# Kernel optimization log

Hardware: AMD Instinct MI355X
Metric: run time of the kernel (lower is better)

## Reference

```python
import jax, jax.numpy as jnp
import numpy as np

H = 2        # num_heads
C = 128      # in_channels
K_ORDER = 4
BETA = 0.5


def _gcn_conv(x, row, col, deg_inv, n):
    # x: [N, H, C]; adj_t = D^{-1} A^T where A[row, col] = 1
    # (adj_t @ x)[c] = deg_inv[c] * sum_{e: col_e == c} x[row_e]
    msg = x[row]  # [E, H, C]
    agg = jax.ops.segment_sum(msg, col, num_segments=n)  # [N, H, C]
    return agg * deg_inv[:, None, None]


def _attn_conv(qs, ks, vs):
    # linear (kernelized) attention, non-block path
    n = qs.shape[0]
    kvs = jnp.einsum('lhm,lhd->hmd', ks, vs)            # [H, C, C]
    qkvs = jnp.einsum('nhm,hmd->nhd', qs, kvs)          # [N, H, C]
    vs_sum = vs.sum(axis=0)                             # [H, C]
    num = qkvs + vs_sum[None, :, :]
    ks_sum = ks.sum(axis=0)                             # [H, C]
    qks_sum = jnp.einsum('nhm,hm->nh', qs, ks_sum)[:, :, None]  # [N, H, 1]
    den = qks_sum + jnp.asarray(n, qs.dtype)
    return num / den


def setup_inputs() -> dict:
    key = jax.random.key(0)
    ks = jax.random.split(key, 8)
    N, E = 100000, 1600000
    x = jax.random.normal(ks[0], (N, C), jnp.float32)
    edge_index = jax.random.randint(ks[1], (2, E), 0, N, jnp.int64)
    s_in = 1.0 / np.sqrt(C)
    s_out = 1.0 / np.sqrt(H * C * (K_ORDER + 1))
    Wq_w = jax.random.normal(ks[2], (C, H * C), jnp.float32) * s_in
    Wq_b = jax.random.normal(ks[3], (H * C,), jnp.float32) * s_in
    Wk_w = jax.random.normal(ks[4], (C, H * C), jnp.float32) * s_in
    Wk_b = jax.random.normal(ks[5], (H * C,), jnp.float32) * s_in
    Wo_w = jax.random.normal(ks[6], (H * C * (K_ORDER + 1), C), jnp.float32) * s_out
    Wo_b = jax.random.normal(ks[7], (C,), jnp.float32) * s_out
    return {"x": x, "edge_index": edge_index, "Wq_w": Wq_w, "Wq_b": Wq_b,
            "Wk_w": Wk_w, "Wk_b": Wk_b, "Wo_w": Wo_w, "Wo_b": Wo_b}


def reference(x, edge_index, Wq_w, Wq_b, Wk_w, Wk_b, Wo_w, Wo_b):
    n = x.shape[0]
    row, col = edge_index[0], edge_index[1]
    # normalized adjacency D^{-1} A^T (pow(-1.0) in the source, not -0.5)
    deg = jax.ops.segment_sum(jnp.ones(row.shape[0], x.dtype), col, num_segments=n)
    deg_inv = jnp.where(deg > 0, 1.0 / deg, 0.0)

    query = (x @ Wq_w + Wq_b).reshape(n, H, C)
    key = (x @ Wk_w + Wk_b).reshape(n, H, C)
    qs = query / jnp.linalg.norm(query, axis=2, keepdims=True)
    ks = key / jnp.linalg.norm(key, axis=2, keepdims=True)

    x0 = jnp.broadcast_to(x[:, None, :], (n, H, C))  # [N, H, C]
    terms = [x0]
    for _ in range(K_ORDER):
        prev = terms[-1]
        gcn_i = _gcn_conv(prev, row, col, deg_inv, n)
        attn_i = _attn_conv(qs, ks, prev)
        terms.append(BETA * gcn_i + attn_i)
    xcat = jnp.concatenate(terms, axis=-1)  # [N, H, C*(K+1)]
    xcat = xcat.reshape(n, H * C * (K_ORDER + 1))
    return (xcat @ Wo_w + Wo_b) / H
```

## Files before the change

### kernel.cpp

```cpp
#include <hip/hip_runtime.h>

#define THREADS 256
#define NB 512
#define SEGCAP 6144

typedef __attribute__((ext_vector_type(8))) short short8;
typedef __attribute__((ext_vector_type(4))) float f32x4;

__device__ __forceinline__ float bf2f(unsigned short u) {
    union { unsigned int i; float f; } v;
    v.i = ((unsigned int)u) << 16;
    return v.f;
}
__device__ __forceinline__ unsigned short f2bf(float f) {
    union { float f; unsigned int i; } v;
    v.f = f;
    unsigned int r = (v.i + 0x7FFFu + ((v.i >> 16) & 1u)) >> 16;
    return (unsigned short)r;
}
__device__ __forceinline__ float4 ld4f(const float* p) {
    return *reinterpret_cast<const float4*>(p);
}
__device__ __forceinline__ float4 ld4f(const unsigned short* p) {
    ushort4 u = *reinterpret_cast<const ushort4*>(p);
    return make_float4(bf2f(u.x), bf2f(u.y), bf2f(u.z), bf2f(u.w));
}

__device__ __forceinline__ int edge_get(const int* base, int E, int mode, int which, int e) {
    size_t idx = (size_t)which * (size_t)E + (size_t)e;
    return mode ? base[2 * idx] : base[idx];
}

__global__ __launch_bounds__(256) void k_detect(const int* __restrict__ e, int E,
                                                int* __restrict__ mode) {
    __shared__ int nz;
    if (threadIdx.x == 0) nz = 0;
    __syncthreads();
    int lim = 2 * E;
    if (lim > 8192) lim = 8192;
    for (int i = 1 + 2 * (int)threadIdx.x; i < lim; i += 512)
        if (e[i] != 0) nz = 1;
    __syncthreads();
    if (threadIdx.x == 0) *mode = (nz == 0) ? 1 : 0;
}

__global__ __launch_bounds__(256) void k_hist(const int* __restrict__ eb, int E,
                                              const int* __restrict__ mode, int N, int CW, int epb,
                                              int* __restrict__ gcnt) {
    __shared__ int hist[NB];
    for (int i = threadIdx.x; i < NB; i += 256) hist[i] = 0;
    __syncthreads();
    int m = *mode;
    int e0 = blockIdx.x * epb;
    int e1 = min(e0 + epb, E);
    for (int e = e0 + threadIdx.x; e < e1; e += 256) {
        int c = edge_get(eb, E, m, 1, e);
        if ((unsigned)c < (unsigned)N) atomicAdd(&hist[c / CW], 1);
    }
    __syncthreads();
    for (int i = threadIdx.x; i < NB; i += 256)
        if (hist[i]) atomicAdd(&gcnt[i], hist[i]);
}

__global__ __launch_bounds__(NB) void k_bscan(const int* __restrict__ gcnt,
                                              int* __restrict__ gbase, int* __restrict__ gcursor) {
    __shared__ int s[NB];
    int t = threadIdx.x;
    int v = gcnt[t];
    s[t] = v;
    __syncthreads();
    for (int off = 1; off < NB; off <<= 1) {
        int add = (t >= off) ? s[t - off] : 0;
        __syncthreads();
        s[t] += add;
        __syncthreads();
    }
    gbase[t] = s[t] - v;
    gcursor[t] = s[t] - v;
}

__global__ __launch_bounds__(256) void k_part(const int* __restrict__ eb, int E,
                                              const int* __restrict__ mode, int N, int CW, int epb,
                                              int* __restrict__ gcursor, uint2* __restrict__ ebuf) {
    __shared__ int hist[NB];
    __shared__ int base[NB];
    for (int i = threadIdx.x; i < NB; i += 256) hist[i] = 0;
    __syncthreads();
    int m = *mode;
    int e0 = blockIdx.x * epb;
    int e1 = min(e0 + epb, E);
    for (int e = e0 + threadIdx.x; e < e1; e += 256) {
        int c = edge_get(eb, E, m, 1, e);
        if ((unsigned)c < (unsigned)N) atomicAdd(&hist[c / CW], 1);
    }
    __syncthreads();
    for (int i = threadIdx.x; i < NB; i += 256) {
        int h = hist[i];
        base[i] = h ? atomicAdd(&gcursor[i], h) : 0;
        hist[i] = 0;
    }
    __syncthreads();
    for (int e = e0 + threadIdx.x; e < e1; e += 256) {
        int c = edge_get(eb, E, m, 1, e);
        if ((unsigned)c < (unsigned)N) {
            int r = edge_get(eb, E, m, 0, e);
            if ((unsigned)r >= (unsigned)N) r = 0;
            int b = c / CW;
            int li = atomicAdd(&hist[b], 1);
            ebuf[(size_t)base[b] + li] = make_uint2((unsigned)r, (unsigned)c);
        }
    }
}

__global__ __launch_bounds__(256) void k_build(const uint2* __restrict__ ebuf,
                                               const int* __restrict__ gbase,
                                               const int* __restrict__ gcnt, int N, int CW,
                                               int* __restrict__ cnt, int* __restrict__ offs,
                                               float* __restrict__ deg_inv, int* __restrict__ csr) {
    __shared__ int hist[256];
    __shared__ int pfx[256];
    __shared__ int seg[SEGCAP];
    const int b = blockIdx.x;
    const int col0 = b * CW;
    const int ncols = min(CW, N - col0);
    if (ncols <= 0) return;
    const int ebase = gbase[b], ecnt = gcnt[b];
    const int t = threadIdx.x;
    for (int i = t; i < 256; i += 256) hist[i] = 0;
    __syncthreads();
    for (int e = t; e < ecnt; e += 256) {
        uint2 rc = ebuf[(size_t)ebase + e];
        atomicAdd(&hist[rc.y - col0], 1);
    }
    __syncthreads();
    int v = (t < ncols) ? hist[t] : 0;
    pfx[t] = v;
    __syncthreads();
    for (int off = 1; off < 256; off <<= 1) {
        int add = (t >= off) ? pfx[t - off] : 0;
        __syncthreads();
        pfx[t] += add;
        __syncthreads();
    }
    int excl = pfx[t] - v;
    if (t < ncols) {
        cnt[col0 + t] = v;
        offs[col0 + t] = ebase + excl;
        deg_inv[col0 + t] = (v > 0) ? 1.0f / (float)v : 0.0f;
    }
    __syncthreads();
    if (t < 256) hist[t] = (t < ncols) ? excl : 0;
    __syncthreads();
    if (ecnt <= SEGCAP) {
        for (int e = t; e < ecnt; e += 256) {
            uint2 rc = ebuf[(size_t)ebase + e];
            int li = atomicAdd(&hist[rc.y - col0], 1);
            seg[li] = (int)rc.x;
        }
        __syncthreads();
        for (int e = t; e < ecnt; e += 256) csr[(size_t)ebase + e] = seg[e];
    } else {
        for (int e = t; e < ecnt; e += 256) {
            uint2 rc = ebuf[(size_t)ebase + e];
            int li = atomicAdd(&hist[rc.y - col0], 1);
            csr[(size_t)ebase + li] = (int)rc.x;
        }
    }
}

__global__ __launch_bounds__(256) void k_prep_wqk(const float* __restrict__ Wq,
                                                  const float* __restrict__ Wk,
                                                  unsigned short* __restrict__ WqkT) {
    int i = blockIdx.x * 256 + threadIdx.x;
    if (i < 512 * 128) {
        int oc = i >> 7, k = i & 127;
        float v = (oc < 256) ? Wq[k * 256 + oc] : Wk[k * 256 + (oc - 256)];
        WqkT[i] = f2bf(v);
    }
}

__global__ __launch_bounds__(256) void k_prep_wo(const float* __restrict__ Wo,
                                                 unsigned short* __restrict__ WoT) {
    int i = blockIdx.x * 256 + threadIdx.x;
    if (i < 1280 * 128) {
        int r = i >> 7, j = i & 127;
        WoT[(size_t)j * 1280 + r] = f2bf(Wo[i]);
    }
}

__global__ __launch_bounds__(256) void k_proj(const float* __restrict__ x,
                                              const unsigned short* __restrict__ WqkT,
                                              const float* __restrict__ bq,
                                              const float* __restrict__ bk,
                                              unsigned short* __restrict__ qs,
                                              unsigned short* __restrict__ ks, int N) {
    __shared__ unsigned short xs[64 * 128];
    __shared__ unsigned short os[64 * 256];
    const int t = threadIdx.x;
    const int n0 = blockIdx.x * 64;
#pragma unroll
    for (int i = 0; i < 4; i++) {
        int chunk = i * 256 + t;
        int r = chunk >> 4, c0 = (chunk & 15) * 8;
        float4 a0 = make_float4(0.f, 0.f, 0.f, 0.f), a1 = a0;
        if (n0 + r < N) {
            a0 = ld4f(&x[(size_t)(n0 + r) * 128 + c0]);
            a1 = ld4f(&x[(size_t)(n0 + r) * 128 + c0 + 4]);
        }
        short8 v = {(short)f2bf(a0.x), (short)f2bf(a0.y), (short)f2bf(a0.z), (short)f2bf(a0.w),
                    (short)f2bf(a1.x), (short)f2bf(a1.y), (short)f2bf(a1.z), (short)f2bf(a1.w)};
        int byte = r * 256 + ((c0 * 2) ^ ((r & 7) << 4));
        *reinterpret_cast<short8*>(reinterpret_cast<char*>(xs) + byte) = v;
    }
    __syncthreads();
    const int w = t >> 6, l = t & 63, lrow = l & 15, lhi = l >> 4;
    f32x4 acc[4][8];
    const f32x4 fz = {0.f, 0.f, 0.f, 0.f};
#pragma unroll
    for (int mt = 0; mt < 4; mt++)
#pragma unroll
        for (int nt = 0; nt < 8; nt++) acc[mt][nt] = fz;

    for (int kk = 0; kk < 4; kk++) {
        int kb = kk * 32 + lhi * 8;
        short8 af[4];
#pragma unroll
        for (int mt = 0; mt < 4; mt++) {
            int r = mt * 16 + lrow;
            af[mt] = *reinterpret_cast<const short8*>(
                reinterpret_cast<const char*>(xs) + r * 256 + ((kb * 2) ^ ((r & 7) << 4)));
        }
#pragma unroll
        for (int nt = 0; nt < 8; nt++) {
            int oc = w * 128 + nt * 16 + lrow;
            short8 bf = *reinterpret_cast<const short8*>(&WqkT[(size_t)oc * 128 + kb]);
#pragma unroll
            for (int mt = 0; mt < 4; mt++)
                acc[mt][nt] = __builtin_amdgcn_mfma_f32_16x16x32_bf16(af[mt], bf, acc[mt][nt], 0, 0, 0);
        }
    }
#pragma unroll
    for (int nt = 0; nt < 8; nt++) {
        int oc = w * 128 + nt * 16 + lrow;
        float b = (oc < 256) ? bq[oc] : bk[oc - 256];
#pragma unroll
        for (int mt = 0; mt < 4; mt++)
#pragma unroll
            for (int reg = 0; reg < 4; reg++) acc[mt][nt][reg] += b;
    }
    const int hc = (w & 1) * 128;
    float rv[4][4];
#pragma unroll
    for (int mt = 0; mt < 4; mt++) {
        float ss[4] = {0.f, 0.f, 0.f, 0.f};
#pragma unroll
        for (int nt = 0; nt < 8; nt++)
#pragma unroll
            for (int reg = 0; reg < 4; reg++) ss[reg] += acc[mt][nt][reg] * acc[mt][nt][reg];
#pragma unroll
        for (int m_ = 1; m_ < 16; m_ <<= 1)
#pragma unroll
            for (int reg = 0; reg < 4; reg++) ss[reg] += __shfl_xor(ss[reg], m_);
#pragma unroll
        for (int reg = 0; reg < 4; reg++) rv[mt][reg] = rsqrtf(ss[reg]);
    }
    for (int pass = 0; pass < 2; pass++) {
        if ((w >> 1) == pass) {
#pragma unroll
            for (int mt = 0; mt < 4; mt++)
#pragma unroll
                for (int reg = 0; reg < 4; reg++) {
                    int r = mt * 16 + lhi * 4 + reg;
#pragma unroll
                    for (int nt = 0; nt < 8; nt++)
                        os[r * 256 + hc + nt * 16 + lrow] = f2bf(acc[mt][nt][reg] * rv[mt][reg]);
                }
        }
        __syncthreads();
        unsigned short* dstg = pass ? ks : qs;
#pragma unroll
        for (int i = 0; i < 8; i++) {
            int chunk = i * 256 + t;
            int r = chunk >> 5, c = (chunk & 31) * 8;
            int n = n0 + r;
            if (n < N)
                *reinterpret_cast<short8*>(&dstg[(size_t)n * 256 + c]) =
                    *reinterpret_cast<const short8*>(&os[r * 256 + c]);
        }
        __syncthreads();
    }
}

__global__ __launch_bounds__(256) void k_colsum(const unsigned short* __restrict__ ks, int N,
                                                float* __restrict__ part) {
    const int t = threadIdx.x;
    const int stride = (N + 255) >> 8;
    int r0 = blockIdx.x * stride;
    int rend = min(r0 + stride, N);
    float s = 0.f;
    for (int n = r0; n < rend; n++) s += bf2f(ks[(size_t)n * 256 + t]);
    part[blockIdx.x * 256 + t] = s;
}

__global__ __launch_bounds__(256) void k_colsum2(const float* __restrict__ part,
                                                 float* __restrict__ ks_sum) {
    const int t = threadIdx.x;
    float s = 0.f;
    for (int b = 0; b < 256; b++) s += part[b * 256 + t];
    ks_sum[t] = s;
}

__global__ __launch_bounds__(256) void k_den(const unsigned short* __restrict__ qs,
                                             const float* __restrict__ ks_sum,
                                             float* __restrict__ den, int N) {
    int w = threadIdx.x >> 6, lane = threadIdx.x & 63;
    int n = blockIdx.x * 4 + w;
    if (n >= N) return;
    float4 q = ld4f(&qs[(size_t)n * 256 + lane * 4]);
    float4 kv = *reinterpret_cast<const float4*>(&ks_sum[lane * 4]);
    float s = q.x * kv.x + q.y * kv.y + q.z * kv.z + q.w * kv.w;
#pragma unroll
    for (int off = 1; off < 32; off <<= 1) s += __shfl_xor(s, off);
    if ((lane & 31) == 0) den[n * 2 + (lane >> 5)] = s + (float)N;
}

__device__ __forceinline__ short8 frag_ld(const unsigned short* tile, int kb, int col) {
    const char* b = reinterpret_cast<const char*>(tile);
    int cb = (col * 2) ^ (((kb >> 3) & 3) << 5);
    short8 r;
#pragma unroll
    for (int i = 0; i < 8; i++)
        r[i] = (short)*reinterpret_cast<const unsigned short*>(b + (kb + i) * 512 + cb);
    return r;
}

template <typename TV>
__global__ __launch_bounds__(256) void k_kvs2(const unsigned short* __restrict__ ks,
                                              const TV* __restrict__ vs, int vstride, int vmask,
                                              float* __restrict__ partial,
                                              float* __restrict__ pvsum, int rows_per, int N) {
    __shared__ unsigned short kt[32 * 256];
    __shared__ unsigned short vt[32 * 256];
    __shared__ float vred[8][256];
    const int t = threadIdx.x;
    const int w = t >> 6, l = t & 63, lrow = l & 15, lhi = l >> 4;
    const int h = w >> 1, mhalf = w & 1;
    const int r0 = blockIdx.x * rows_per;
    const int rend = min(r0 + rows_per, N);

    const f32x4 fz = {0.f, 0.f, 0.f, 0.f};
    f32x4 acc[4][8];
#pragma unroll
    for (int mt = 0; mt < 4; mt++)
#pragma unroll
        for (int nt = 0; nt < 8; nt++) acc[mt][nt] = fz;
    float vsum8[8] = {0.f, 0.f, 0.f, 0.f, 0.f, 0.f, 0.f, 0.f};

    for (int c0 = r0; c0 < rend; c0 += 32) {
#pragma unroll
        for (int i = 0; i < 4; i++) {
            int chunk = i * 256 + t;
            int n = chunk >> 5, cc = (chunk & 31) * 8;
            short8 v = {0, 0, 0, 0, 0, 0, 0, 0};
            if (c0 + n < rend)
                v = *reinterpret_cast<const short8*>(&ks[(size_t)(c0 + n) * 256 + cc]);
            *reinterpret_cast<short8*>(reinterpret_cast<char*>(kt) + n * 512 +
                                       ((cc * 2) ^ (((n >> 3) & 3) << 5))) = v;
        }
#pragma unroll
        for (int i = 0; i < 4; i++) {
            int chunk = i * 256 + t;
            int n = chunk >> 5, cc = (chunk & 31) * 8;
            float4 a0 = make_float4(0.f, 0.f, 0.f, 0.f), a1 = a0;
            if (c0 + n < rend) {
                a0 = ld4f(&vs[(size_t)(c0 + n) * vstride + (cc & vmask)]);
                a1 = ld4f(&vs[(size_t)(c0 + n) * vstride + ((cc + 4) & vmask)]);
            }
            unsigned short u0 = f2bf(a0.x), u1 = f2bf(a0.y), u2 = f2bf(a0.z), u3 = f2bf(a0.w);
            unsigned short u4 = f2bf(a1.x), u5 = f2bf(a1.y), u6 = f2bf(a1.z), u7 = f2bf(a1.w);
            vsum8[0] += bf2f(u0); vsum8[1] += bf2f(u1); vsum8[2] += bf2f(u2); vsum8[3] += bf2f(u3);
            vsum8[4] += bf2f(u4); vsum8[5] += bf2f(u5); vsum8[6] += bf2f(u6); vsum8[7] += bf2f(u7);
            short8 v = {(short)u0, (short)u1, (short)u2, (short)u3,
                        (short)u4, (short)u5, (short)u6, (short)u7};
            *reinterpret_cast<short8*>(reinterpret_cast<char*>(vt) + n * 512 +
                                       ((cc * 2) ^ (((n >> 3) & 3) << 5))) = v;
        }
        __syncthreads();
        {
            int kb = lhi * 8;
            short8 af[4];
#pragma unroll
            for (int mt = 0; mt < 4; mt++)
                af[mt] = frag_ld(vt, kb, h * 128 + mhalf * 64 + mt * 16 + lrow);
#pragma unroll
            for (int nt = 0; nt < 8; nt++) {
                short8 bf = frag_ld(kt, kb, h * 128 + nt * 16 + lrow);
#pragma unroll
                for (int mt = 0; mt < 4; mt++)
                    acc[mt][nt] =
                        __builtin_amdgcn_mfma_f32_16x16x32_bf16(af[mt], bf, acc[mt][nt], 0, 0, 0);
            }
        }
        __syncthreads();
    }
    float* pb = &partial[((size_t)blockIdx.x * 2 + h) * 16384];
#pragma unroll
    for (int mt = 0; mt < 4; mt++)
#pragma unroll
        for (int reg = 0; reg < 4; reg++) {
            int c_local = mhalf * 64 + mt * 16 + lhi * 4 + reg;
#pragma unroll
            for (int nt = 0; nt < 8; nt++) pb[c_local * 128 + nt * 16 + lrow] = acc[mt][nt][reg];
        }
    {
        int cc = (t & 31) * 8;
#pragma unroll
        for (int j = 0; j < 8; j++) vred[t >> 5][cc + j] = vsum8[j];
        __syncthreads();
        float s = 0.f;
#pragma unroll
        for (int r = 0; r < 8; r++) s += vred[r][t];
        pvsum[blockIdx.x * 256 + t] = s;
    }
}

__global__ __launch_bounds__(256) void k_kvred(const float* __restrict__ partial,
                                               const float* __restrict__ pvsum, int S,
                                               unsigned short* __restrict__ kvsT,
                                               float* __restrict__ vs_sum) {
    if (blockIdx.x == 128) {
        int c = threadIdx.x;
        float s = 0.f;
        for (int i = 0; i < S; i++) s += pvsum[i * 256 + c];
        vs_sum[c] = s;
        return;
    }
    int e = blockIdx.x * 256 + threadIdx.x;
    float s = 0.f;
    for (int i = 0; i < S; i++) s += partial[(size_t)i * 32768 + e];
    kvsT[e] = f2bf(s);
}

__global__ __launch_bounds__(256) void k_gather2(const unsigned short* __restrict__ prev,
                                                 const int* __restrict__ csr_src,
                                                 const int* __restrict__ offs,
                                                 const int* __restrict__ cnt,
                                                 const float* __restrict__ deg_inv,
                                                 unsigned short* __restrict__ cur, int N) {
    const int w = threadIdx.x >> 6, l = threadIdx.x & 63;
    int n = blockIdx.x * 4 + w;
    if (n >= N) return;
    const int start = offs[n], d = cnt[n];
    int e = start;
    const int eend = start + d;
    float a0 = 0.f, a1 = 0.f, a2 = 0.f, a3 = 0.f;
    const int co = l * 4;
    for (; e + 8 <= eend; e += 8) {
        int s[8];
#pragma unroll
        for (int i = 0; i < 8; i++) s[i] = csr_src[e + i];
        ushort4 u[8];
#pragma unroll
        for (int i = 0; i < 8; i++)
            u[i] = *reinterpret_cast<const ushort4*>(&prev[(size_t)s[i] * 256 + co]);
#pragma unroll
        for (int i = 0; i < 8; i++) {
            a0 += bf2f(u[i].x); a1 += bf2f(u[i].y); a2 += bf2f(u[i].z); a3 += bf2f(u[i].w);
        }
    }
    for (; e < eend; e++) {
        ushort4 u = *reinterpret_cast<const ushort4*>(&prev[(size_t)csr_src[e] * 256 + co]);
        a0 += bf2f(u.x); a1 += bf2f(u.y); a2 += bf2f(u.z); a3 += bf2f(u.w);
    }
    float sc = 0.5f * deg_inv[n];
    ushort4 o;
    o.x = f2bf(a0 * sc); o.y = f2bf(a1 * sc); o.z = f2bf(a2 * sc); o.w = f2bf(a3 * sc);
    *reinterpret_cast<ushort4*>(&cur[(size_t)n * 256 + co]) = o;
}

__global__ __launch_bounds__(256) void k_gather2f(const float* __restrict__ prev,
                                                  const int* __restrict__ csr_src,
                                                  const int* __restrict__ offs,
                                                  const int* __restrict__ cnt,
                                                  const float* __restrict__ deg_inv,
                                                  unsigned short* __restrict__ cur, int N) {
    const int w = threadIdx.x >> 6, l = threadIdx.x & 63;
    int n = blockIdx.x * 4 + w;
    if (n >= N) return;
    const int start = offs[n], d = cnt[n];
    int e = start;
    const int eend = start + d;
    float a0 = 0.f, a1 = 0.f;
    const int co = l * 2;
    for (; e + 8 <= eend; e += 8) {
        int s[8];
#pragma unroll
        for (int i = 0; i < 8; i++) s[i] = csr_src[e + i];
        float2 u[8];
#pragma unroll
        for (int i = 0; i < 8; i++)
            u[i] = *reinterpret_cast<const float2*>(&prev[(size_t)s[i] * 128 + co]);
#pragma unroll
        for (int i = 0; i < 8; i++) { a0 += u[i].x; a1 += u[i].y; }
    }
    for (; e < eend; e++) {
        float2 u = *reinterpret_cast<const float2*>(&prev[(size_t)csr_src[e] * 128 + co]);
        a0 += u.x; a1 += u.y;
    }
    float sc = 0.5f * deg_inv[n];
    ushort2 o;
    o.x = f2bf(a0 * sc); o.y = f2bf(a1 * sc);
    *reinterpret_cast<ushort2*>(&cur[(size_t)n * 256 + co]) = o;
    *reinterpret_cast<ushort2*>(&cur[(size_t)n * 256 + 128 + co]) = o;
}

__global__ __launch_bounds__(256) void k_att_out(const unsigned short* __restrict__ qs,
                                                 const unsigned short* __restrict__ kvsT,
                                                 const float* __restrict__ vs_sum,
                                                 const float* __restrict__ den,
                                                 unsigned short* __restrict__ cur,
                                                 const unsigned short* __restrict__ WoT,
                                                 float* __restrict__ out, int tblk, int N) {
    __shared__ unsigned short sm[64 * 256];
    const int t = threadIdx.x;
    const int n0 = blockIdx.x * 64;
#pragma unroll
    for (int i = 0; i < 8; i++) {
        int chunk = i * 256 + t;
        int r = chunk >> 5, c0 = (chunk & 31) * 8;
        short8 v = {0, 0, 0, 0, 0, 0, 0, 0};
        if (n0 + r < N) v = *reinterpret_cast<const short8*>(&qs[(size_t)(n0 + r) * 256 + c0]);
        *reinterpret_cast<short8*>(reinterpret_cast<char*>(sm) + r * 512 +
                                   ((c0 * 2) ^ ((r & 7) << 4))) = v;
    }
    __syncthreads();
    const int w = t >> 6, l = t & 63, lrow = l & 15, lhi = l >> 4;
    const int h = w >> 1, jh = w & 1;
    const f32x4 fz = {0.f, 0.f, 0.f, 0.f};
    f32x4 acc[4][4];
#pragma unroll
    for (int mt = 0; mt < 4; mt++)
#pragma unroll
        for (int nt = 0; nt < 4; nt++) acc[mt][nt] = fz;

    for (int kk = 0; kk < 4; kk++) {
        int kb = kk * 32 + lhi * 8;
        short8 af[4];
#pragma unroll
        for (int mt = 0; mt < 4; mt++) {
            int r = mt * 16 + lrow;
            af[mt] = *reinterpret_cast<const short8*>(
                reinterpret_cast<const char*>(sm) + r * 512 +
                (((h * 128 + kb) * 2) ^ ((r & 7) << 4)));
        }
#pragma unroll
        for (int nt = 0; nt < 4; nt++) {
            int c = jh * 64 + nt * 16 + lrow;
            short8 bf = *reinterpret_cast<const short8*>(&kvsT[((size_t)h * 128 + c) * 128 + kb]);
#pragma unroll
            for (int mt = 0; mt < 4; mt++)
                acc[mt][nt] = __builtin_amdgcn_mfma_f32_16x16x32_bf16(af[mt], bf, acc[mt][nt], 0, 0, 0);
        }
    }
    __syncthreads();
#pragma unroll
    for (int i = 0; i < 8; i++) {
        int chunk = i * 256 + t;
        int r = chunk >> 5, c0 = (chunk & 31) * 8;
        short8 v = {0, 0, 0, 0, 0, 0, 0, 0};
        if (n0 + r < N) v = *reinterpret_cast<const short8*>(&cur[(size_t)(n0 + r) * 256 + c0]);
        *reinterpret_cast<short8*>(reinterpret_cast<char*>(sm) + r * 512 +
                                   ((c0 * 2) ^ ((r & 7) << 4))) = v;
    }
    __syncthreads();
#pragma unroll
    for (int mt = 0; mt < 4; mt++) {
#pragma unroll
        for (int reg = 0; reg < 4; reg++) {
            int r = mt * 16 + lhi * 4 + reg;
            int n = n0 + r;
            if (n < N) {
                float idn = 1.0f / den[n * 2 + h];
#pragma unroll
                for (int nt = 0; nt < 4; nt++) {
                    int c = h * 128 + jh * 64 + nt * 16 + lrow;
                    unsigned short* sp = reinterpret_cast<unsigned short*>(
                        reinterpret_cast<char*>(sm) + r * 512 + ((c * 2) ^ ((r & 7) << 4)));
                    float v = bf2f(*sp) + (acc[mt][nt][reg] + vs_sum[c]) * idn;
                    *sp = f2bf(v);
                }
            }
        }
    }
    __syncthreads();
#pragma unroll
    for (int i = 0; i < 8; i++) {
        int chunk = i * 256 + t;
        int r = chunk >> 5, c0 = (chunk & 31) * 8;
        int n = n0 + r;
        if (n < N)
            *reinterpret_cast<short8*>(&cur[(size_t)n * 256 + c0]) =
                *reinterpret_cast<const short8*>(reinterpret_cast<const char*>(sm) + r * 512 +
                                                 ((c0 * 2) ^ ((r & 7) << 4)));
    }
    __syncthreads();
    f32x4 acc2[4][2];
#pragma unroll
    for (int mt = 0; mt < 4; mt++)
#pragma unroll
        for (int nt = 0; nt < 2; nt++) acc2[mt][nt] = fz;
    for (int kk = 0; kk < 8; kk++) {
        int kb = kk * 32 + lhi * 8;
        short8 af[4];
#pragma unroll
        for (int mt = 0; mt < 4; mt++) {
            int r = mt * 16 + lrow;
            af[mt] = *reinterpret_cast<const short8*>(
                reinterpret_cast<const char*>(sm) + r * 512 + ((kb * 2) ^ ((r & 7) << 4)));
        }
        int woff = (kb >> 7) * 640 + tblk * 128 + (kb & 127);
#pragma unroll
        for (int nt = 0; nt < 2; nt++) {
            int j = w * 32 + nt * 16 + lrow;
            short8 bf = *reinterpret_cast<const short8*>(&WoT[(size_t)j * 1280 + woff]);
#pragma unroll
            for (int mt = 0; mt < 4; mt++)
                acc2[mt][nt] = __builtin_amdgcn_mfma_f32_16x16x32_bf16(af[mt], bf, acc2[mt][nt], 0, 0, 0);
        }
    }
#pragma unroll
    for (int nt = 0; nt < 2; nt++) {
        int j = w * 32 + nt * 16 + lrow;
#pragma unroll
        for (int mt = 0; mt < 4; mt++)
#pragma unroll
            for (int reg = 0; reg < 4; reg++) {
                int n = n0 + mt * 16 + lhi * 4 + reg;
                if (n < N) out[(size_t)n * 128 + j] += 0.5f * acc2[mt][nt][reg];
            }
    }
}

__global__ __launch_bounds__(256) void k_out0(const float* __restrict__ x,
                                              const unsigned short* __restrict__ WoT,
                                              const float* __restrict__ Wo_b,
                                              float* __restrict__ out, int N) {
    __shared__ unsigned short sm[64 * 256];
    const int t = threadIdx.x;
    const int n0 = blockIdx.x * 64;
#pragma unroll
    for (int i = 0; i < 8; i++) {
        int chunk = i * 256 + t;
        int r = chunk >> 5, c0 = (chunk & 31) * 8, cs = c0 & 127;
        float4 a0 = make_float4(0.f, 0.f, 0.f, 0.f), a1 = a0;
        if (n0 + r < N) {
            a0 = ld4f(&x[(size_t)(n0 + r) * 128 + cs]);
            a1 = ld4f(&x[(size_t)(n0 + r) * 128 + cs + 4]);
        }
        short8 v = {(short)f2bf(a0.x), (short)f2bf(a0.y), (short)f2bf(a0.z), (short)f2bf(a0.w),
                    (short)f2bf(a1.x), (short)f2bf(a1.y), (short)f2bf(a1.z), (short)f2bf(a1.w)};
        *reinterpret_cast<short8*>(reinterpret_cast<char*>(sm) + r * 512 +
                                   ((c0 * 2) ^ ((r & 7) << 4))) = v;
    }
    __syncthreads();
    const int w = t >> 6, l = t & 63, lrow = l & 15, lhi = l >> 4;
    const f32x4 fz = {0.f, 0.f, 0.f, 0.f};
    f32x4 acc2[4][2];
#pragma unroll
    for (int mt = 0; mt < 4; mt++)
#pragma unroll
        for (int nt = 0; nt < 2; nt++) acc2[mt][nt] = fz;
    for (int kk = 0; kk < 8; kk++) {
        int kb = kk * 32 + lhi * 8;
        short8 af[4];
#pragma unroll
        for (int mt = 0; mt < 4; mt++) {
            int r = mt * 16 + lrow;
            af[mt] = *reinterpret_cast<const short8*>(
                reinterpret_cast<const char*>(sm) + r * 512 + ((kb * 2) ^ ((r & 7) << 4)));
        }
        int woff = (kb >> 7) * 640 + (kb & 127);
#pragma unroll
        for (int nt = 0; nt < 2; nt++) {
            int j = w * 32 + nt * 16 + lrow;
            short8 bf = *reinterpret_cast<const short8*>(&WoT[(size_t)j * 1280 + woff]);
#pragma unroll
            for (int mt = 0; mt < 4; mt++)
                acc2[mt][nt] = __builtin_amdgcn_mfma_f32_16x16x32_bf16(af[mt], bf, acc2[mt][nt], 0, 0, 0);
        }
    }
#pragma unroll
    for (int nt = 0; nt < 2; nt++) {
        int j = w * 32 + nt * 16 + lrow;
        float b = Wo_b[j];
#pragma unroll
        for (int mt = 0; mt < 4; mt++)
#pragma unroll
            for (int reg = 0; reg < 4; reg++) {
                int n = n0 + mt * 16 + lhi * 4 + reg;
                if (n < N) out[(size_t)n * 128 + j] = 0.5f * (acc2[mt][nt][reg] + b);
            }
    }
}

extern "C" void kernel_launch(void* const* d_in, const int* in_sizes, int n_in,
                              void* d_out, int out_size, void* d_ws, size_t ws_size,
                              hipStream_t stream) {
    const int N = in_sizes[0] / 128;
    const int E = in_sizes[1] / 2;
    const float* x = (const float*)d_in[0];
    const int* eraw = (const int*)d_in[1];
    const float* Wq_w = (const float*)d_in[2];
    const float* Wq_b = (const float*)d_in[3];
    const float* Wk_w = (const float*)d_in[4];
    const float* Wk_b = (const float*)d_in[5];
    const float* Wo_w = (const float*)d_in[6];
    const float* Wo_b = (const float*)d_in[7];
    float* out = (float*)d_out;

    char* p = (char*)d_ws;
    auto alloc = [&](size_t bytes) -> void* {
        void* r = (void*)p;
        p += (bytes + 255) & ~(size_t)255;
        return r;
    };
    unsigned short* qs = (unsigned short*)alloc((size_t)N * 256 * 2);
    unsigned short* ks = (unsigned short*)alloc((size_t)N * 256 * 2);
    unsigned short* bufA = (unsigned short*)alloc((size_t)N * 256 * 2);
    unsigned short* bufB = (unsigned short*)alloc((size_t)N * 256 * 2);
    float* deg_inv = (float*)alloc((size_t)N * 4);
    float* den = (float*)alloc((size_t)N * 2 * 4);
    float* ks_sum = (float*)alloc(256 * 4);
    float* vs_sum = (float*)alloc(256 * 4);
    float* colpart = (float*)alloc(256 * 256 * 4);
    unsigned short* WqkT = (unsigned short*)alloc(512 * 128 * 2);
    unsigned short* WoT = (unsigned short*)alloc(1280 * 128 * 2);
    unsigned short* kvsTb = (unsigned short*)alloc(32768 * 2);
    int* cnt = (int*)alloc((size_t)N * 4);
    int* offs = (int*)alloc((size_t)N * 4);
    int* gcnt = (int*)alloc(NB * 4);
    int* gbase = (int*)alloc(NB * 4);
    int* gcursor = (int*)alloc(NB * 4);
    int* mode = (int*)alloc(256);
    int* csr = (int*)alloc((size_t)E * 4);
    uint2* ebuf = (uint2*)alloc((size_t)E * 8);

    size_t used = (size_t)(p - (char*)d_ws);
    size_t rem = (ws_size > used + (1 << 20)) ? ws_size - used - (1 << 20) : 0;
    int S = (int)(rem / (32768 * 4 + 1024));
    if (S > 256) S = 256;
    if (S < 8) S = 8;
    float* partial = (float*)alloc((size_t)S * 32768 * 4);
    float* pvsum = (float*)alloc((size_t)S * 256 * 4);
    const int rows_per = (N + S - 1) / S;

    const int CW = (N + NB - 1) / NB;
    const int EBLK = 256;
    const int epb = (E + EBLK - 1) / EBLK;

    hipMemsetAsync(gcnt, 0, NB * 4, stream);

    k_detect<<<1, 256, 0, stream>>>(eraw, E, mode);
    k_hist<<<EBLK, 256, 0, stream>>>(eraw, E, mode, N, CW, epb, gcnt);
    k_bscan<<<1, NB, 0, stream>>>(gcnt, gbase, gcursor);
    k_part<<<EBLK, 256, 0, stream>>>(eraw, E, mode, N, CW, epb, gcursor, ebuf);
    k_build<<<NB, 256, 0, stream>>>(ebuf, gbase, gcnt, N, CW, cnt, offs, deg_inv, csr);

    k_prep_wqk<<<256, 256, 0, stream>>>(Wq_w, Wk_w, WqkT);
    k_prep_wo<<<640, 256, 0, stream>>>(Wo_w, WoT);

    const int nb64 = (N + 63) / 64;
    k_proj<<<nb64, 256, 0, stream>>>(x, WqkT, Wq_b, Wk_b, qs, ks, N);
    k_colsum<<<256, 256, 0, stream>>>(ks, N, colpart);
    k_colsum2<<<1, 256, 0, stream>>>(colpart, ks_sum);
    k_den<<<(N + 3) / 4, 256, 0, stream>>>(qs, ks_sum, den, N);
    k_out0<<<nb64, 256, 0, stream>>>(x, WoT, Wo_b, out, N);

    const int gb4 = (N + 3) / 4;

    k_kvs2<float><<<S, 256, 0, stream>>>(ks, x, 128, 127, partial, pvsum, rows_per, N);
    k_kvred<<<129, 256, 0, stream>>>(partial, pvsum, S, kvsTb, vs_sum);
    k_gather2f<<<gb4, 256, 0, stream>>>(x, csr, offs, cnt, deg_inv, bufA, N);
    k_att_out<<<nb64, 256, 0, stream>>>(qs, kvsTb, vs_sum, den, bufA, WoT, out, 1, N);

    unsigned short* prev = bufA;
    unsigned short* cur = bufB;
    for (int step = 2; step <= 4; step++) {
        k_kvs2<unsigned short><<<S, 256, 0, stream>>>(ks, prev, 256, 255, partial, pvsum, rows_per,
                                                      N);
        k_kvred<<<129, 256, 0, stream>>>(partial, pvsum, S, kvsTb, vs_sum);
        k_gather2<<<gb4, 256, 0, stream>>>(prev, csr, offs, cnt, deg_inv, cur, N);
        k_att_out<<<nb64, 256, 0, stream>>>(qs, kvsTb, vs_sum, den, cur, WoT, out, step, N);
        unsigned short* tmp = prev;
        prev = cur;
        cur = tmp;
    }
}
```

Baseline: 1.795 ms.

## Unroll gathers deeper, prefetch cur in att_out, skip final write-back, raise split cap

Adds a 16-edge unrolled loop to both GCN gather kernels so more independent row loads are in flight per wavefront. In the attention/output kernel the cur tile is now loaded into registers before the first MFMA phase, overlapping that global read with compute. The kernel no longer writes the updated term back to global memory on the last order, since nothing reads it. The cap on the KV reduction split count rises from 256 to 512. The costs are higher register pressure from the wider unroll and the prefetch buffer, and more partial sums for the reduction kernel to combine.

```diff
diff --git a/kernel.cpp b/kernel.cpp
--- a/kernel.cpp
+++ b/kernel.cpp
@@ -455,6 +455,19 @@
     const int eend = start + d;
     float a0 = 0.f, a1 = 0.f, a2 = 0.f, a3 = 0.f;
     const int co = l * 4;
+    for (; e + 16 <= eend; e += 16) {
+        int s[16];
+#pragma unroll
+        for (int i = 0; i < 16; i++) s[i] = csr_src[e + i];
+        ushort4 u[16];
+#pragma unroll
+        for (int i = 0; i < 16; i++)
+            u[i] = *reinterpret_cast<const ushort4*>(&prev[(size_t)s[i] * 256 + co]);
+#pragma unroll
+        for (int i = 0; i < 16; i++) {
+            a0 += bf2f(u[i].x); a1 += bf2f(u[i].y); a2 += bf2f(u[i].z); a3 += bf2f(u[i].w);
+        }
+    }
     for (; e + 8 <= eend; e += 8) {
         int s[8];
 #pragma unroll
@@ -492,6 +505,17 @@
     const int eend = start + d;
     float a0 = 0.f, a1 = 0.f;
     const int co = l * 2;
+    for (; e + 16 <= eend; e += 16) {
+        int s[16];
+#pragma unroll
+        for (int i = 0; i < 16; i++) s[i] = csr_src[e + i];
+        float2 u[16];
+#pragma unroll
+        for (int i = 0; i < 16; i++)
+            u[i] = *reinterpret_cast<const float2*>(&prev[(size_t)s[i] * 128 + co]);
+#pragma unroll
+        for (int i = 0; i < 16; i++) { a0 += u[i].x; a1 += u[i].y; }
+    }
     for (; e + 8 <= eend; e += 8) {
         int s[8];
 #pragma unroll
@@ -520,7 +544,8 @@
                                                  const float* __restrict__ den,
                                                  unsigned short* __restrict__ cur,
                                                  const unsigned short* __restrict__ WoT,
-                                                 float* __restrict__ out, int tblk, int N) {
+                                                 float* __restrict__ out, int tblk, int writeCur,
+                                                 int N) {
     __shared__ unsigned short sm[64 * 256];
     const int t = threadIdx.x;
     const int n0 = blockIdx.x * 64;
@@ -533,6 +558,15 @@
         *reinterpret_cast<short8*>(reinterpret_cast<char*>(sm) + r * 512 +
                                    ((c0 * 2) ^ ((r & 7) << 4))) = v;
     }
+    short8 cv[8];
+#pragma unroll
+    for (int i = 0; i < 8; i++) {
+        int chunk = i * 256 + t;
+        int r = chunk >> 5, c0 = (chunk & 31) * 8;
+        short8 v = {0, 0, 0, 0, 0, 0, 0, 0};
+        if (n0 + r < N) v = *reinterpret_cast<const short8*>(&cur[(size_t)(n0 + r) * 256 + c0]);
+        cv[i] = v;
+    }
     __syncthreads();
     const int w = t >> 6, l = t & 63, lrow = l & 15, lhi = l >> 4;
     const int h = w >> 1, jh = w & 1;
@@ -567,10 +601,8 @@
     for (int i = 0; i < 8; i++) {
         int chunk = i * 256 + t;
         int r = chunk >> 5, c0 = (chunk & 31) * 8;
-        short8 v = {0, 0, 0, 0, 0, 0, 0, 0};
-        if (n0 + r < N) v = *reinterpret_cast<const short8*>(&cur[(size_t)(n0 + r) * 256 + c0]);
         *reinterpret_cast<short8*>(reinterpret_cast<char*>(sm) + r * 512 +
-                                   ((c0 * 2) ^ ((r & 7) << 4))) = v;
+                                   ((c0 * 2) ^ ((r & 7) << 4))) = cv[i];
     }
     __syncthreads();
 #pragma unroll
@@ -593,17 +625,18 @@
         }
     }
     __syncthreads();
-#pragma unroll
-    for (int i = 0; i < 8; i++) {
-        int chunk = i * 256 + t;
-        int r = chunk >> 5, c0 = (chunk & 31) * 8;
-        int n = n0 + r;
-        if (n < N)
-            *reinterpret_cast<short8*>(&cur[(size_t)n * 256 + c0]) =
-                *reinterpret_cast<const short8*>(reinterpret_cast<const char*>(sm) + r * 512 +
-                                                 ((c0 * 2) ^ ((r & 7) << 4)));
-    }
-    __syncthreads();
+    if (writeCur) {
+#pragma unroll
+        for (int i = 0; i < 8; i++) {
+            int chunk = i * 256 + t;
+            int r = chunk >> 5, c0 = (chunk & 31) * 8;
+            int n = n0 + r;
+            if (n < N)
+                *reinterpret_cast<short8*>(&cur[(size_t)n * 256 + c0]) =
+                    *reinterpret_cast<const short8*>(reinterpret_cast<const char*>(sm) + r * 512 +
+                                                     ((c0 * 2) ^ ((r & 7) << 4)));
+        }
+    }
     f32x4 acc2[4][2];
 #pragma unroll
     for (int mt = 0; mt < 4; mt++)
@@ -748,7 +781,7 @@
     size_t used = (size_t)(p - (char*)d_ws);
     size_t rem = (ws_size > used + (1 << 20)) ? ws_size - used - (1 << 20) : 0;
     int S = (int)(rem / (32768 * 4 + 1024));
-    if (S > 256) S = 256;
+    if (S > 512) S = 512;
     if (S < 8) S = 8;
     float* partial = (float*)alloc((size_t)S * 32768 * 4);
     float* pvsum = (float*)alloc((size_t)S * 256 * 4);
@@ -781,7 +814,7 @@
     k_kvs2<float><<<S, 256, 0, stream>>>(ks, x, 128, 127, partial, pvsum, rows_per, N);
     k_kvred<<<129, 256, 0, stream>>>(partial, pvsum, S, kvsTb, vs_sum);
     k_gather2f<<<gb4, 256, 0, stream>>>(x, csr, offs, cnt, deg_inv, bufA, N);
-    k_att_out<<<nb64, 256, 0, stream>>>(qs, kvsTb, vs_sum, den, bufA, WoT, out, 1, N);
+    k_att_out<<<nb64, 256, 0, stream>>>(qs, kvsTb, vs_sum, den, bufA, WoT, out, 1, 1, N);
 
     unsigned short* prev = bufA;
     unsigned short* cur = bufB;
@@ -790,7 +823,8 @@
                                                       N);
         k_kvred<<<129, 256, 0, stream>>>(partial, pvsum, S, kvsTb, vs_sum);
         k_gather2<<<gb4, 256, 0, stream>>>(prev, csr, offs, cnt, deg_inv, cur, N);
-        k_att_out<<<nb64, 256, 0, stream>>>(qs, kvsTb, vs_sum, den, cur, WoT, out, step, N);
+        k_att_out<<<nb64, 256, 0, stream>>>(qs, kvsTb, vs_sum, den, cur, WoT, out, step,
+                                            (step < 4) ? 1 : 0, N);
         unsigned short* tmp = prev;
         prev = cur;
         cur = tmp;
```

New measurement: 1.857 ms. +3.4%, slower.
